# Kernel optimization log

Hardware: AMD Instinct MI355X
Metric: run time of the kernel (lower is better)

Reference implementation:

```python
import jax, jax.numpy as jnp
import numpy as np

B, S, E = 4, 2048, 768
H = 12
D = E // H  # 64

def setup_inputs() -> dict:
    key = jax.random.key(0)
    k_x, k_wqkv, k_wproj = jax.random.split(key, 3)
    x = jax.random.normal(k_x, (B, S, E), dtype=jnp.float32)
    w_qkv = jax.random.normal(k_wqkv, (E, 3 * E), dtype=jnp.float32) * 0.02
    b_qkv = jnp.zeros((3 * E,), dtype=jnp.float32)
    w_proj = jax.random.normal(k_wproj, (E, E), dtype=jnp.float32) * 0.02
    b_proj = jnp.zeros((E,), dtype=jnp.float32)
    return {"x": x, "w_qkv": w_qkv, "b_qkv": b_qkv, "w_proj": w_proj, "b_proj": b_proj}

def reference(x, w_qkv, b_qkv, w_proj, b_proj):
    # fused QKV projection: [B,S,E] -> [B,S,3E]
    qkv = jnp.einsum("bse,ef->bsf", x, w_qkv) + b_qkv
    qkv = qkv.reshape(B, S, 3, H, D)
    q, k, v = qkv[:, :, 0], qkv[:, :, 1], qkv[:, :, 2]  # [B,S,H,D]
    scale = 1.0 / jnp.sqrt(jnp.asarray(D, dtype=x.dtype))
    # causal scaled dot-product attention (explicit score matrix, as in module)
    scores = jnp.einsum("bshd,bthd->bhst", q, k) * scale  # [B,H,S,S]
    causal = jnp.tril(jnp.ones((S, S), dtype=bool))
    scores = jnp.where(causal, scores, jnp.finfo(scores.dtype).min)
    probs = jax.nn.softmax(scores, axis=-1)
    attn = jnp.einsum("bhst,bthd->bshd", probs, v).reshape(B, S, E)
    # output projection
    out = jnp.einsum("bse,ef->bsf", attn, w_proj) + b_proj
    return out
```

## Files before the change

kernel.cpp:

```cpp
#include <hip/hip_runtime.h>

#define SDIM 2048
#define EDIM 768
#define HDIM 12
#define DDIM 64
#define BDIM 4
#define MROWS (BDIM * SDIM)
#define NQKV (3 * EDIM)
#define NBH (BDIM * HDIM)
#define NTILE 32
#define NPAIR 16

typedef __attribute__((ext_vector_type(8))) short s16x8;
typedef __attribute__((ext_vector_type(4))) float f32x4;
typedef __attribute__((ext_vector_type(2))) unsigned int u32x2;

__device__ __forceinline__ short f2b(float x) {
  union { float f; unsigned u; } v; v.f = x;
  unsigned r = v.u + 0x7fffu + ((v.u >> 16) & 1u);
  return (short)(r >> 16);
}

__device__ __forceinline__ unsigned cvtpk(float lo, float hi) {
  unsigned r;
  asm volatile("v_cvt_pk_bf16_f32 %0, %1, %2" : "=v"(r) : "v"(lo), "v"(hi));
  return r;
}

__device__ __forceinline__ float fexp2(float x) {
  float r;
  asm("v_exp_f32 %0, %1" : "=v"(r) : "v"(x));
  return r;
}

__device__ __forceinline__ void gld16(const void* g, void* l) {
  __builtin_amdgcn_global_load_lds(
      (const __attribute__((address_space(1))) unsigned int*)g,
      (__attribute__((address_space(3))) unsigned int*)l, 16, 0, 0);
}

__global__ __launch_bounds__(256) void convert_bf16(
    const float* __restrict__ in, short* __restrict__ out, int n4) {
  int i = blockIdx.x * 256 + threadIdx.x;
  int stride = gridDim.x * 256;
  for (; i < n4; i += stride) {
    float4 v = ((const float4*)in)[i];
    short4 o;
    o.x = f2b(v.x); o.y = f2b(v.y); o.z = f2b(v.z); o.w = f2b(v.w);
    ((short4*)out)[i] = o;
  }
}

__global__ __launch_bounds__(256) void transpose_bf16(
    const float* __restrict__ in, short* __restrict__ out, int K, int N) {
  __shared__ float t[32][33];
  int n0 = blockIdx.x * 32, k0 = blockIdx.y * 32;
  int tx = threadIdx.x & 31, ty = threadIdx.x >> 5;
#pragma unroll
  for (int i = 0; i < 4; ++i)
    t[ty + 8 * i][tx] = in[(size_t)(k0 + ty + 8 * i) * N + n0 + tx];
  __syncthreads();
#pragma unroll
  for (int i = 0; i < 4; ++i)
    out[(size_t)(n0 + ty + 8 * i) * K + k0 + tx] = f2b(t[tx][ty + 8 * i]);
}

__global__ __launch_bounds__(256) void gemm_bf16(
    const short* __restrict__ A, const short* __restrict__ Bt,
    const float* __restrict__ bias, int M, int N, int K, int mode,
    short* __restrict__ qout, short* __restrict__ kout,
    short* __restrict__ vout, float* __restrict__ fout) {
  __shared__ char lds[3][16384];
  const int tid = threadIdx.x;
  const int l = tid & 63, w = tid >> 6;
  const int lr = l & 15, g = l >> 4;
  const int bm = blockIdx.y * 128, bn = blockIdx.x * 128;
  const int wm = w >> 1, wn = w & 1;

  const int srow = w * 32 + (l >> 2);
  const int sc8 = (((l & 3) ^ ((l >> 3) & 3)) << 3);
  const short* Ap0 = A + (size_t)(bm + srow) * K + sc8;
  const short* Bp0 = Bt + (size_t)(bn + srow) * K + sc8;

  f32x4 acc[4][4];
  const f32x4 z4 = {0.f, 0.f, 0.f, 0.f};
#pragma unroll
  for (int m = 0; m < 4; ++m)
#pragma unroll
    for (int n = 0; n < 4; ++n) acc[m][n] = z4;

#define STAGE(dst, t)                          \
  {                                            \
    char* Ad = (dst) + w * 2048;               \
    const short* Ap = Ap0 + (t) * 32;          \
    const short* Bp = Bp0 + (t) * 32;          \
    gld16(Ap, Ad);                             \
    gld16(Ap + 16 * K, Ad + 1024);             \
    gld16(Bp, Ad + 8192);                      \
    gld16(Bp + 16 * K, Ad + 9216);             \
  }

  const int nt = K >> 5;
  STAGE(lds[0], 0);
  STAGE(lds[1], 1);
  asm volatile("s_waitcnt vmcnt(4)" ::: "memory");
  __builtin_amdgcn_s_barrier();

  const int swz = ((lr >> 1) & 3) << 4;
  int bc = 0;
  for (int t = 0; t < nt; ++t) {
    if (t + 2 < nt) {
      int bs = bc + 2; if (bs >= 3) bs -= 3;
      STAGE(lds[bs], t + 2);
    }
    const char* Ab = lds[bc];
    const char* Bb = lds[bc] + 8192;
    s16x8 af[4], bfr[4];
#pragma unroll
    for (int m = 0; m < 4; ++m)
      af[m] = *(const s16x8*)(Ab + (wm * 64 + m * 16 + lr) * 64 + ((g << 4) ^ swz));
#pragma unroll
    for (int n = 0; n < 4; ++n)
      bfr[n] = *(const s16x8*)(Bb + (wn * 64 + n * 16 + lr) * 64 + ((g << 4) ^ swz));
#pragma unroll
    for (int m = 0; m < 4; ++m)
#pragma unroll
      for (int n = 0; n < 4; ++n)
        acc[m][n] = __builtin_amdgcn_mfma_f32_16x16x32_bf16(af[m], bfr[n],
                                                            acc[m][n], 0, 0, 0);
    if (t + 2 < nt) {
      asm volatile("s_waitcnt vmcnt(4)" ::: "memory");
      __builtin_amdgcn_s_barrier();
    } else if (t + 1 < nt) {
      asm volatile("s_waitcnt vmcnt(0)" ::: "memory");
      __builtin_amdgcn_s_barrier();
    }
    if (++bc == 3) bc = 0;
  }
#undef STAGE

#pragma unroll
  for (int m = 0; m < 4; ++m) {
    int rbase = bm + wm * 64 + m * 16 + g * 4;
#pragma unroll
    for (int n = 0; n < 4; ++n) {
      int col = bn + wn * 64 + n * 16 + lr;
      float bv = bias[col];
      if (mode == 0) {
        int which = (col >= 1536) ? 2 : (col >= 768 ? 1 : 0);
        int rem = col - which * 768;
        int h = rem >> 6, d = rem & 63;
#pragma unroll
        for (int i = 0; i < 4; ++i) {
          int r = rbase + i;
          int b = r >> 11, s = r & 2047;
          short o = f2b(acc[m][n][i] + bv);
          size_t bh = (size_t)b * HDIM + h;
          if (which == 0)      qout[(bh * SDIM + s) * DDIM + d] = o;
          else if (which == 1) kout[(bh * SDIM + s) * DDIM + d] = o;
          else                 vout[(bh * DDIM + d) * SDIM + s] = o;
        }
      } else {
#pragma unroll
        for (int i = 0; i < 4; ++i)
          fout[(size_t)(rbase + i) * N + col] = acc[m][n][i] + bv;
      }
    }
  }
}

__global__ __launch_bounds__(256) void attn_mfma3(
    const short* __restrict__ qb, const short* __restrict__ kb,
    const short* __restrict__ vb, short* __restrict__ ao) {
  __shared__ short kvbuf[2][8192];
  __shared__ short pstrip[4][1024];

  const int tid = threadIdx.x;
  const int l = tid & 63, w = tid >> 6;
  const int lr = l & 15, g = l >> 4;
  const int swz = (lr & 7) << 4;

  const int lin = blockIdx.x;
  const int xcd = lin & 7;
  const int idx = lin >> 3;
  const int bh = xcd * 6 + (idx >> 4);
  const int pair = idx & 15;
  const int tiles[2] = {NTILE - 1 - pair, pair};

  const int b = bh / HDIM, h = bh % HDIM;
  const size_t base = (size_t)bh * SDIM * DDIM;

  const int srow = w * 16 + (l >> 3);
  const int sc = (l & 7) ^ (srow & 7);
  const size_t koff0 = (size_t)srow * DDIM + sc * 8;
  const size_t koff1 = (size_t)(srow + 8) * DDIM + sc * 8;
  const size_t voff0 = (size_t)srow * SDIM + sc * 8;
  const size_t voff1 = (size_t)(srow + 8) * SDIM + sc * 8;

  const float SC = 0.125f * 1.4426950408889634f;
  char* sw = (char*)pstrip[w];

  for (int half = 0; half < 2; ++half) {
    const int tile = tiles[half];
    const int q0w = tile * 64 + w * 16;

    s16x8 qa[2];
#pragma unroll
    for (int s = 0; s < 2; ++s)
      qa[s] = *(const s16x8*)(qb + base + (size_t)(q0w + lr) * DDIM + s * 32 + g * 8);

    const f32x4 z4 = {0.f, 0.f, 0.f, 0.f};
    f32x4 acco[4];
#pragma unroll
    for (int nd = 0; nd < 4; ++nd) acco[nd] = z4;
    float mrun = -1e30f, lsum = 0.f;

    int cur = 0;
    {
      char* kd = (char*)kvbuf[cur] + w * 2048;
      const short* kp = kb + base;
      const short* vp = vb + base;
      gld16(kp + koff0, kd);
      gld16(kp + koff1, kd + 1024);
      gld16(vp + voff0, kd + 8192);
      gld16(vp + voff1, kd + 9216);
    }
    __syncthreads();

    for (int kt = 0; kt <= tile; ++kt) {
      if (kt < tile) {
        char* kd = (char*)kvbuf[cur ^ 1] + w * 2048;
        const short* kp = kb + base + (size_t)(kt + 1) * 64 * DDIM;
        const short* vp = vb + base + (size_t)(kt + 1) * 64;
        gld16(kp + koff0, kd);
        gld16(kp + koff1, kd + 1024);
        gld16(vp + voff0, kd + 8192);
        gld16(vp + voff1, kd + 9216);
      }

      const char* Kb = (const char*)kvbuf[cur];
      const char* Vb = Kb + 8192;

      f32x4 sacc[4];
#pragma unroll
      for (int nt = 0; nt < 4; ++nt) sacc[nt] = z4;
      __builtin_amdgcn_s_setprio(1);
#pragma unroll
      for (int s = 0; s < 2; ++s)
#pragma unroll
        for (int nt = 0; nt < 4; ++nt) {
          s16x8 kf = *(const s16x8*)(Kb + nt * 2048 + lr * 128 +
                                     ((s * 64 + g * 16) ^ swz));
          sacc[nt] = __builtin_amdgcn_mfma_f32_16x16x32_bf16(kf, qa[s],
                                                             sacc[nt], 0, 0, 0);
        }
      __builtin_amdgcn_s_setprio(0);

      if (kt == tile) {
        const int rloc = w * 16 + lr;
#pragma unroll
        for (int nt = 0; nt < 4; ++nt)
#pragma unroll
          for (int i = 0; i < 4; ++i)
            if (nt * 16 + g * 4 + i > rloc) sacc[nt][i] = -1e30f;
      }

      float t0 = fmaxf(fmaxf(sacc[0][0], sacc[0][1]), fmaxf(sacc[0][2], sacc[0][3]));
      float t1 = fmaxf(fmaxf(sacc[1][0], sacc[1][1]), fmaxf(sacc[1][2], sacc[1][3]));
      float t2 = fmaxf(fmaxf(sacc[2][0], sacc[2][1]), fmaxf(sacc[2][2], sacc[2][3]));
      float t3 = fmaxf(fmaxf(sacc[3][0], sacc[3][1]), fmaxf(sacc[3][2], sacc[3][3]));
      float pmax = fmaxf(fmaxf(t0, t1), fmaxf(t2, t3));
      pmax = fmaxf(pmax, __shfl_xor(pmax, 16, 64));
      pmax = fmaxf(pmax, __shfl_xor(pmax, 32, 64));

      if (__any(pmax > mrun + 44.0f)) {
        float nm = fmaxf(mrun, pmax);
        float al = fexp2((mrun - nm) * SC);
        lsum *= al;
#pragma unroll
        for (int nd = 0; nd < 4; ++nd)
#pragma unroll
          for (int i = 0; i < 4; ++i) acco[nd][i] *= al;
        mrun = nm;
      }

      const float msc = mrun * SC;
#pragma unroll
      for (int nt = 0; nt < 4; ++nt) {
        float p0 = fexp2(__builtin_fmaf(sacc[nt][0], SC, -msc));
        float p1 = fexp2(__builtin_fmaf(sacc[nt][1], SC, -msc));
        float p2 = fexp2(__builtin_fmaf(sacc[nt][2], SC, -msc));
        float p3 = fexp2(__builtin_fmaf(sacc[nt][3], SC, -msc));
        lsum += (p0 + p1) + (p2 + p3);
        u32x2 pk = {cvtpk(p0, p1), cvtpk(p2, p3)};
        *(u32x2*)(sw + lr * 128 + (((nt * 32 + g * 8) ^ swz))) = pk;
      }

      __builtin_amdgcn_s_setprio(1);
#pragma unroll
      for (int s = 0; s < 2; ++s) {
        s16x8 pf = *(const s16x8*)(sw + lr * 128 + ((s * 64 + g * 16) ^ swz));
#pragma unroll
        for (int nd = 0; nd < 4; ++nd) {
          s16x8 vf = *(const s16x8*)(Vb + nd * 2048 + lr * 128 +
                                     ((s * 64 + g * 16) ^ swz));
          acco[nd] = __builtin_amdgcn_mfma_f32_16x16x32_bf16(vf, pf,
                                                             acco[nd], 0, 0, 0);
        }
      }
      __builtin_amdgcn_s_setprio(0);

      __syncthreads();
      cur ^= 1;
    }

    lsum += __shfl_xor(lsum, 16, 64);
    lsum += __shfl_xor(lsum, 32, 64);
    float inv = 1.0f / lsum;
    size_t orow = ((size_t)b * SDIM + q0w + lr) * EDIM + h * DDIM;
#pragma unroll
    for (int nd = 0; nd < 4; ++nd) {
      unsigned lo = cvtpk(acco[nd][0] * inv, acco[nd][1] * inv);
      unsigned hi = cvtpk(acco[nd][2] * inv, acco[nd][3] * inv);
      *(unsigned*)(ao + orow + nd * 16 + g * 4) = lo;
      *(unsigned*)(ao + orow + nd * 16 + g * 4 + 2) = hi;
    }
  }
}

extern "C" void kernel_launch(void* const* d_in, const int* in_sizes, int n_in,
                              void* d_out, int out_size, void* d_ws,
                              size_t ws_size, hipStream_t stream) {
  const float* x = (const float*)d_in[0];
  const float* w_qkv = (const float*)d_in[1];
  const float* b_qkv = (const float*)d_in[2];
  const float* w_proj = (const float*)d_in[3];
  const float* b_proj = (const float*)d_in[4];
  float* out = (float*)d_out;

  char* p = (char*)d_ws;
  short* xb = (short*)p;      p += (size_t)MROWS * EDIM * 2;
  short* wqkvt = (short*)p;   p += (size_t)NQKV * EDIM * 2;
  short* wprojt = (short*)p;  p += (size_t)EDIM * EDIM * 2;
  short* qbuf = (short*)p;    p += (size_t)NBH * SDIM * DDIM * 2;
  short* kbuf = (short*)p;    p += (size_t)NBH * SDIM * DDIM * 2;
  short* vbuf = (short*)p;    p += (size_t)NBH * SDIM * DDIM * 2;
  short* aob = (short*)p;     p += (size_t)MROWS * EDIM * 2;

  dim3 blk(256);
  convert_bf16<<<dim3(2048), blk, 0, stream>>>(x, xb, MROWS * EDIM / 4);
  transpose_bf16<<<dim3(NQKV / 32, EDIM / 32), blk, 0, stream>>>(w_qkv, wqkvt, EDIM, NQKV);
  transpose_bf16<<<dim3(EDIM / 32, EDIM / 32), blk, 0, stream>>>(w_proj, wprojt, EDIM, EDIM);
  gemm_bf16<<<dim3(NQKV / 128, MROWS / 128), blk, 0, stream>>>(
      xb, wqkvt, b_qkv, MROWS, NQKV, EDIM, 0, qbuf, kbuf, vbuf, nullptr);
  attn_mfma3<<<dim3(NPAIR * NBH), blk, 0, stream>>>(qbuf, kbuf, vbuf, aob);
  gemm_bf16<<<dim3(EDIM / 128, MROWS / 128), blk, 0, stream>>>(
      aob, wprojt, b_proj, MROWS, EDIM, EDIM, 1, nullptr, nullptr, nullptr, out);
}
```

Measured before the change: 151.1 us.

## Fuse preprocessing kernels, XCD-aware GEMM block remap, raise MFMA priority

Merges the x bf16 conversion and the two weight transposes into one preproc launch, which removes two kernel launches and the gaps between them. Switches the GEMM grid to 1D and remaps block IDs so consecutive tiles land on the same XCD (chunked by 8), aiming for better L2 reuse of A/B tiles. Wraps the MFMA loop in s_setprio to favor the compute waves. Together these are three unrelated tweaks, and the remap assumes the grid size divides evenly by 8.

After: 140.0 us. 7.3% less time.

```diff
diff --git a/kernel.cpp b/kernel.cpp
--- a/kernel.cpp
+++ b/kernel.cpp
@@ -39,30 +39,36 @@
       (__attribute__((address_space(3))) unsigned int*)l, 16, 0, 0);
 }
 
-__global__ __launch_bounds__(256) void convert_bf16(
-    const float* __restrict__ in, short* __restrict__ out, int n4) {
-  int i = blockIdx.x * 256 + threadIdx.x;
-  int stride = gridDim.x * 256;
-  for (; i < n4; i += stride) {
-    float4 v = ((const float4*)in)[i];
-    short4 o;
-    o.x = f2b(v.x); o.y = f2b(v.y); o.z = f2b(v.z); o.w = f2b(v.w);
-    ((short4*)out)[i] = o;
-  }
-}
-
-__global__ __launch_bounds__(256) void transpose_bf16(
-    const float* __restrict__ in, short* __restrict__ out, int K, int N) {
-  __shared__ float t[32][33];
-  int n0 = blockIdx.x * 32, k0 = blockIdx.y * 32;
+__global__ __launch_bounds__(256) void preproc(
+    const float* __restrict__ x, const float* __restrict__ wqkv,
+    const float* __restrict__ wproj, short* __restrict__ xb,
+    short* __restrict__ wqkvt, short* __restrict__ wprojt) {
+  int bid = blockIdx.x;
+  if (bid < 1536) {
+    int i = bid * 256 + threadIdx.x;
+    const int n4 = MROWS * EDIM / 4;
+    for (; i < n4; i += 1536 * 256) {
+      float4 v = ((const float4*)x)[i];
+      short4 o;
+      o.x = f2b(v.x); o.y = f2b(v.y); o.z = f2b(v.z); o.w = f2b(v.w);
+      ((short4*)xb)[i] = o;
+    }
+    return;
+  }
+  const float* in; short* out; int K, N, t;
+  if (bid < 1536 + 1728) { t = bid - 1536; in = wqkv; out = wqkvt; K = EDIM; N = NQKV; }
+  else { t = bid - 1536 - 1728; in = wproj; out = wprojt; K = EDIM; N = EDIM; }
+  const int ntx = N / 32;
+  int n0 = (t % ntx) * 32, k0 = (t / ntx) * 32;
+  __shared__ float tb[32][33];
   int tx = threadIdx.x & 31, ty = threadIdx.x >> 5;
 #pragma unroll
   for (int i = 0; i < 4; ++i)
-    t[ty + 8 * i][tx] = in[(size_t)(k0 + ty + 8 * i) * N + n0 + tx];
+    tb[ty + 8 * i][tx] = in[(size_t)(k0 + ty + 8 * i) * N + n0 + tx];
   __syncthreads();
 #pragma unroll
   for (int i = 0; i < 4; ++i)
-    out[(size_t)(n0 + ty + 8 * i) * K + k0 + tx] = f2b(t[tx][ty + 8 * i]);
+    out[(size_t)(n0 + ty + 8 * i) * K + k0 + tx] = f2b(tb[tx][ty + 8 * i]);
 }
 
 __global__ __launch_bounds__(256) void gemm_bf16(
@@ -74,7 +80,11 @@
   const int tid = threadIdx.x;
   const int l = tid & 63, w = tid >> 6;
   const int lr = l & 15, g = l >> 4;
-  const int bm = blockIdx.y * 128, bn = blockIdx.x * 128;
+
+  const int chunk = gridDim.x >> 3;
+  const int sid = (blockIdx.x & 7) * chunk + (blockIdx.x >> 3);
+  const int ntx = N >> 7;
+  const int bm = (sid / ntx) * 128, bn = (sid % ntx) * 128;
   const int wm = w >> 1, wn = w & 1;
 
   const int srow = w * 32 + (l >> 2);
@@ -122,12 +132,14 @@
 #pragma unroll
     for (int n = 0; n < 4; ++n)
       bfr[n] = *(const s16x8*)(Bb + (wn * 64 + n * 16 + lr) * 64 + ((g << 4) ^ swz));
+    __builtin_amdgcn_s_setprio(1);
 #pragma unroll
     for (int m = 0; m < 4; ++m)
 #pragma unroll
       for (int n = 0; n < 4; ++n)
         acc[m][n] = __builtin_amdgcn_mfma_f32_16x16x32_bf16(af[m], bfr[n],
                                                             acc[m][n], 0, 0, 0);
+    __builtin_amdgcn_s_setprio(0);
     if (t + 2 < nt) {
       asm volatile("s_waitcnt vmcnt(4)" ::: "memory");
       __builtin_amdgcn_s_barrier();
@@ -348,12 +360,11 @@
   short* aob = (short*)p;     p += (size_t)MROWS * EDIM * 2;
 
   dim3 blk(256);
-  convert_bf16<<<dim3(2048), blk, 0, stream>>>(x, xb, MROWS * EDIM / 4);
-  transpose_bf16<<<dim3(NQKV / 32, EDIM / 32), blk, 0, stream>>>(w_qkv, wqkvt, EDIM, NQKV);
-  transpose_bf16<<<dim3(EDIM / 32, EDIM / 32), blk, 0, stream>>>(w_proj, wprojt, EDIM, EDIM);
-  gemm_bf16<<<dim3(NQKV / 128, MROWS / 128), blk, 0, stream>>>(
+  preproc<<<dim3(1536 + 1728 + 576), blk, 0, stream>>>(x, w_qkv, w_proj, xb,
+                                                       wqkvt, wprojt);
+  gemm_bf16<<<dim3((NQKV / 128) * (MROWS / 128)), blk, 0, stream>>>(
       xb, wqkvt, b_qkv, MROWS, NQKV, EDIM, 0, qbuf, kbuf, vbuf, nullptr);
   attn_mfma3<<<dim3(NPAIR * NBH), blk, 0, stream>>>(qbuf, kbuf, vbuf, aob);
-  gemm_bf16<<<dim3(EDIM / 128, MROWS / 128), blk, 0, stream>>>(
+  gemm_bf16<<<dim3((EDIM / 128) * (MROWS / 128)), blk, 0, stream>>>(
       aob, wprojt, b_proj, MROWS, EDIM, EDIM, 1, nullptr, nullptr, nullptr, out);
 }
```
